# Kernel tuning notes

Hardware: AMD Instinct MI355X
Metric: run time of the kernel (lower is better)

Reference implementation:

```python
import jax, jax.numpy as jnp
import numpy as np

D_MODEL = 1024
N_HEADS = 16
D_HEAD = D_MODEL // N_HEADS
B, T = 4, 2048


def setup_inputs() -> dict:
    key = jax.random.key(0)
    ks = jax.random.split(key, 9)
    s = 0.02
    return {
        "x": jax.random.normal(ks[0], (B, T, D_MODEL), dtype=jnp.float32),
        "Wq": jax.random.normal(ks[1], (D_MODEL, D_MODEL), dtype=jnp.float32) * s,
        "bq": jnp.zeros((D_MODEL,), dtype=jnp.float32),
        "Wk": jax.random.normal(ks[2], (D_MODEL, D_MODEL), dtype=jnp.float32) * s,
        "bk": jnp.zeros((D_MODEL,), dtype=jnp.float32),
        "Wv": jax.random.normal(ks[3], (D_MODEL, D_MODEL), dtype=jnp.float32) * s,
        "bv": jnp.zeros((D_MODEL,), dtype=jnp.float32),
        "Wo": jax.random.normal(ks[4], (D_MODEL, D_MODEL), dtype=jnp.float32) * s,
        "bo": jnp.zeros((D_MODEL,), dtype=jnp.float32),
    }


def reference(x, Wq, bq, Wk, bk, Wv, bv, Wo, bo):
    # Dropout in eval mode (identity), as standard for a correctness baseline.
    Bx, Tx, _ = x.shape
    # torch nn.Linear: y = x @ W.T + b
    Q = x @ Wq.T + bq
    K = x @ Wk.T + bk
    V = x @ Wv.T + bv
    # [B, T, H, Dh] -> [B, H, T, Dh]
    Q = Q.reshape(Bx, Tx, N_HEADS, D_HEAD).transpose(0, 2, 1, 3)
    K = K.reshape(Bx, Tx, N_HEADS, D_HEAD).transpose(0, 2, 1, 3)
    V = V.reshape(Bx, Tx, N_HEADS, D_HEAD).transpose(0, 2, 1, 3)
    scale = 1.0 / jnp.sqrt(jnp.float32(D_HEAD))
    scores = jnp.einsum("bhqd,bhkd->bhqk", Q, K) * scale  # [B,H,T,T]
    # additive causal mask: -1e6 above the diagonal (matches torch.triu trick)
    mask = jnp.triu(jnp.full((Tx, Tx), -1000000.0, dtype=scores.dtype), k=1)
    scores = scores + mask
    attn = jax.nn.softmax(scores, axis=-1)
    out = jnp.einsum("bhqk,bhkd->bhqd", attn, V)  # [B,H,T,Dh]
    out = out.transpose(0, 2, 1, 3).reshape(Bx, Tx, D_MODEL)
    out = out @ Wo.T + bo
    return out
```

## Files before the change

### kernel.cpp

```cpp
#include <hip/hip_runtime.h>
#include <stdint.h>

#define DM 1024
#define HEADS 16
#define DH 64
#define BQ 4
#define TT 2048
#define MTOT (BQ*TT)
#define NQT (TT/64)

typedef __attribute__((ext_vector_type(8))) __bf16 bf16x8;
typedef __attribute__((ext_vector_type(4))) float f32x4;
typedef __attribute__((ext_vector_type(4))) uint32_t u32x4;
typedef unsigned short u16;
typedef __attribute__((ext_vector_type(8))) unsigned short u16x8;

__device__ __forceinline__ u16 f2b(float f) {
  uint32_t u = __builtin_bit_cast(uint32_t, f);
  u = (u + 0x7fffu + ((u >> 16) & 1u)) >> 16;
  return (u16)u;
}

__device__ __forceinline__ uint32_t cvtpk(float lo, float hi) {
  uint32_t r;
  asm("v_cvt_pk_bf16_f32 %0, %1, %2" : "=v"(r) : "v"(lo), "v"(hi));
  return r;
}

__device__ __forceinline__ void gload_lds16(const u16* g, u16* l) {
  __builtin_amdgcn_global_load_lds(
      (const __attribute__((address_space(1))) void*)g,
      (__attribute__((address_space(3))) void*)l, 16, 0, 0);
}

#define NX (MTOT * DM / 4)
#define NW (DM * DM / 4)
__global__ __launch_bounds__(256) void cast_all(const float* __restrict__ x,
                                                const float* __restrict__ Wq,
                                                const float* __restrict__ Wk,
                                                const float* __restrict__ Wv,
                                                const float* __restrict__ Wo,
                                                u16* __restrict__ xb,
                                                u16* __restrict__ wqkvb,
                                                u16* __restrict__ wob) {
  int i = blockIdx.x * 256 + threadIdx.x;
  const float* src; u16* dst;
  if (i < NX)               { src = x;  dst = xb; }
  else if (i < NX + NW)     { src = Wq; dst = wqkvb;          i -= NX; }
  else if (i < NX + 2 * NW) { src = Wk; dst = wqkvb + 4 * NW; i -= NX + NW; }
  else if (i < NX + 3 * NW) { src = Wv; dst = wqkvb + 8 * NW; i -= NX + 2 * NW; }
  else                      { src = Wo; dst = wob;            i -= NX + 3 * NW; }
  float4 v = ((const float4*)src)[i];
  ushort4 o;
  o.x = f2b(v.x); o.y = f2b(v.y); o.z = f2b(v.z); o.w = f2b(v.w);
  ((ushort4*)dst)[i] = o;
}

#define NK2 16
#define SLOT_A2 (256 * 64)
#define SLOT_B2 (128 * 64)
#define SLOT_E2 (SLOT_A2 + SLOT_B2)

__global__ __launch_bounds__(512, 2) void gemm_qkv8(const u16* __restrict__ A,
                                                    const u16* __restrict__ W,
                                                    const float* __restrict__ bq,
                                                    const float* __restrict__ bk,
                                                    const float* __restrict__ bv,
                                                    u16* __restrict__ Qo,
                                                    u16* __restrict__ Ko,
                                                    u16* __restrict__ Vto,
                                                    float qs) {
  __shared__ u16 lds[3 * SLOT_E2];
  const int tid = threadIdx.x, lane = tid & 63, wave = tid >> 6;
  const int fr = lane & 15, g = lane >> 4;
  const int wm = wave >> 1, wn = wave & 1;

  int bid = blockIdx.x;
  bid = (bid & 7) * 96 + (bid >> 3);
  const int by = bid / 24, bx = bid % 24;
  const int m0 = by * 256, n0 = bx * 128;

  const int lr8 = lane >> 3;
  const int lsc = ((lane & 7) ^ lr8) * 8;
  const u16* gA0 = A + (size_t)(m0 + wave * 8 + lr8) * DM + lsc;
  const u16* gB0 = W + (size_t)(n0 + wave * 8 + lr8) * DM + lsc;
  const int dA0 = wave * 512;
  const int dB0 = SLOT_A2 + wave * 512;

#define STAGEQ(ls, kt) {                                     \
    const int ke = (kt) * 64;                                \
    gload_lds16(gA0 + ke,                (ls) + dA0);        \
    gload_lds16(gA0 + ke + (size_t)64  * DM, (ls) + dA0 + 4096);  \
    gload_lds16(gA0 + ke + (size_t)128 * DM, (ls) + dA0 + 8192);  \
    gload_lds16(gA0 + ke + (size_t)192 * DM, (ls) + dA0 + 12288); \
    gload_lds16(gB0 + ke,                (ls) + dB0);        \
    gload_lds16(gB0 + ke + (size_t)64  * DM, (ls) + dB0 + 4096); }

  const int rc0 = ((g) ^ (fr & 7)) * 8;
  const int rc1 = ((4 + g) ^ (fr & 7)) * 8;
  const int offA = (wm * 64 + fr) * 64;
  const int offB = SLOT_A2 + (wn * 64 + fr) * 64;

  f32x4 acc[4][4];
#pragma unroll
  for (int mi = 0; mi < 4; ++mi)
#pragma unroll
    for (int ni = 0; ni < 4; ++ni) acc[mi][ni] = (f32x4){0.f, 0.f, 0.f, 0.f};

  bf16x8 afA[8], bfA[8], afB[8], bfB[8];

#define READQ(AFv, BFv, ls) {                                \
    _Pragma("unroll")                                        \
    for (int mi = 0; mi < 4; ++mi) {                         \
      AFv[2 * mi]     = *(const bf16x8*)&(ls)[offA + mi * 1024 + rc0]; \
      AFv[2 * mi + 1] = *(const bf16x8*)&(ls)[offA + mi * 1024 + rc1]; \
    }                                                        \
    _Pragma("unroll")                                        \
    for (int ni = 0; ni < 4; ++ni) {                         \
      BFv[2 * ni]     = *(const bf16x8*)&(ls)[offB + ni * 1024 + rc0]; \
      BFv[2 * ni + 1] = *(const bf16x8*)&(ls)[offB + ni * 1024 + rc1]; \
    } }

#define MFMAQ(AFv, BFv) {                                    \
    __builtin_amdgcn_s_setprio(1);                           \
    _Pragma("unroll")                                        \
    for (int mi = 0; mi < 4; ++mi)                           \
      _Pragma("unroll")                                      \
      for (int ni = 0; ni < 4; ++ni) {                       \
        acc[mi][ni] = __builtin_amdgcn_mfma_f32_16x16x32_bf16(AFv[2 * mi], BFv[2 * ni], acc[mi][ni], 0, 0, 0); \
        acc[mi][ni] = __builtin_amdgcn_mfma_f32_16x16x32_bf16(AFv[2 * mi + 1], BFv[2 * ni + 1], acc[mi][ni], 0, 0, 0); \
      }                                                      \
    __builtin_amdgcn_s_setprio(0); }

#define QW6 asm volatile("s_waitcnt vmcnt(6)" ::: "memory"); \
            asm volatile("s_barrier" ::: "memory");
#define QW0 asm volatile("s_waitcnt vmcnt(0)" ::: "memory"); \
            asm volatile("s_barrier" ::: "memory");

  u16* p0 = &lds[0];
  u16* p1 = &lds[SLOT_E2];
  u16* p2 = &lds[2 * SLOT_E2];
  u16 *pCur = p0, *pNxt = p1, *pStg = p2;

  STAGEQ(p0, 0)
  STAGEQ(p1, 1)
  asm volatile("s_waitcnt vmcnt(6)" ::: "memory");
  asm volatile("s_barrier" ::: "memory");
  READQ(afA, bfA, p0)

  for (int kt = 0; kt < NK2 - 2; kt += 2) {
    STAGEQ(pStg, kt + 2)
    QW6
    READQ(afB, bfB, pNxt)
    MFMAQ(afA, bfA)
    { u16* t = pCur; pCur = pNxt; pNxt = pStg; pStg = t; }
    if (kt + 3 < NK2) { STAGEQ(pStg, kt + 3) }
    QW6
    READQ(afA, bfA, pNxt)
    MFMAQ(afB, bfB)
    { u16* t = pCur; pCur = pNxt; pNxt = pStg; pStg = t; }
  }
  QW0
  READQ(afB, bfB, pNxt)
  MFMAQ(afA, bfA)
  MFMAQ(afB, bfB)

  const int g4 = g * 4;
  const int seg = n0 >> 10;
  const int nbase = (n0 & 1023) + wn * 64 + fr;
  if (seg == 0) {
#pragma unroll
    for (int ni = 0; ni < 4; ++ni) {
      const int cgl = nbase + ni * 16;
      const float bb = bq[cgl];
      const int hh = cgl >> 6, d = cgl & 63;
#pragma unroll
      for (int mi = 0; mi < 4; ++mi) {
        const int m = m0 + wm * 64 + mi * 16 + g4;
        const int bi = m >> 11, t = m & 2047;
        u16* dst = &Qo[(((size_t)bi * HEADS + hh) * TT + t) * DH + d];
#pragma unroll
        for (int j = 0; j < 4; ++j)
          dst[(size_t)j * DH] = f2b((acc[mi][ni][j] + bb) * qs);
      }
    }
  } else if (seg == 1) {
#pragma unroll
    for (int ni = 0; ni < 4; ++ni) {
      const int cgl = nbase + ni * 16;
      const float bb = bk[cgl];
      const int hh = cgl >> 6, d = cgl & 63;
#pragma unroll
      for (int mi = 0; mi < 4; ++mi) {
        const int m = m0 + wm * 64 + mi * 16 + g4;
        const int bi = m >> 11, t = m & 2047;
        u16* dst = &Ko[(((size_t)bi * HEADS + hh) * TT + t) * DH + d];
#pragma unroll
        for (int j = 0; j < 4; ++j)
          dst[(size_t)j * DH] = f2b(acc[mi][ni][j] + bb);
      }
    }
  } else {
#pragma unroll
    for (int ni = 0; ni < 4; ++ni) {
      const int cgl = nbase + ni * 16;
      const float bb = bv[cgl];
      const int hh = cgl >> 6, d = cgl & 63;
#pragma unroll
      for (int mi = 0; mi < 4; ++mi) {
        const int m = m0 + wm * 64 + mi * 16 + g4;
        const int t0 = m & 2047, bi = m >> 11;
        const int w64 = t0 & 63;
        const int pos = (t0 & ~63) | (((w64 >> 5) & 1) << 5) | (((w64 >> 2) & 3) << 3) |
                        (((w64 >> 4) & 1) << 2);
        ushort4 o;
        o.x = f2b(acc[mi][ni][0] + bb);
        o.y = f2b(acc[mi][ni][1] + bb);
        o.z = f2b(acc[mi][ni][2] + bb);
        o.w = f2b(acc[mi][ni][3] + bb);
        *(ushort4*)&Vto[(((size_t)bi * HEADS + hh) * DH + d) * TT + pos] = o;
      }
    }
  }
#undef STAGEQ
#undef READQ
#undef MFMAQ
#undef QW6
#undef QW0
}

#define SLOT_OA (256 * 32)
#define SLOT_OB (128 * 32)
#define SLOT_OE (SLOT_OA + SLOT_OB)

__global__ __launch_bounds__(512, 2) void gemm_out8(const u16* __restrict__ A,
                                                    const u16* __restrict__ Bw,
                                                    const float* __restrict__ bias,
                                                    float* __restrict__ outp) {
  __shared__ u16 lds[4 * SLOT_OE];
  const int tid = threadIdx.x, lane = tid & 63, wave = tid >> 6;
  const int fr = lane & 15, g = lane >> 4;
  const int wm = wave >> 1, wn = wave & 1;

  const int bx = blockIdx.x >> 5, by = blockIdx.x & 31;
  const int m0 = by * 256, n0 = bx * 128;

  const int srow = tid >> 2;
  const int schunk = (tid & 3) ^ ((tid >> 3) & 3);
  const u16* gA0 = A + (size_t)(m0 + srow) * DM + schunk * 8;
  const u16* gA1 = gA0 + (size_t)128 * DM;
  const u16* gB0 = Bw + (size_t)(n0 + srow) * DM + schunk * 8;
  const int dA0 = wave * 512;
  const int dA1 = 4096 + wave * 512;
  const int dB0 = SLOT_OA + wave * 512;

#define STAGEO(slot, kt) {                                   \
    u16* ls = &lds[(slot) * SLOT_OE];                        \
    const int ke = (kt) * 32;                                \
    gload_lds16(gA0 + ke, ls + dA0);                         \
    gload_lds16(gA1 + ke, ls + dA1);                         \
    gload_lds16(gB0 + ke, ls + dB0); }

  const int rchunk = (g ^ ((fr >> 1) & 3)) * 8;
  const int offA = (wm * 64 + fr) * 32 + rchunk;
  const int offB = SLOT_OA + (wn * 64 + fr) * 32 + rchunk;

  f32x4 acc[4][4];
#pragma unroll
  for (int mi = 0; mi < 4; ++mi)
#pragma unroll
    for (int ni = 0; ni < 4; ++ni) acc[mi][ni] = (f32x4){0.f, 0.f, 0.f, 0.f};

  bf16x8 afA[4], bfA[4], afB[4], bfB[4];

#define READO(AFv, BFv, kt) {                                \
    const u16* sl = &lds[((kt) & 3) * SLOT_OE];              \
    _Pragma("unroll")                                        \
    for (int mi = 0; mi < 4; ++mi)                           \
      AFv[mi] = *(const bf16x8*)&sl[offA + mi * 512];        \
    _Pragma("unroll")                                        \
    for (int ni = 0; ni < 4; ++ni)                           \
      BFv[ni] = *(const bf16x8*)&sl[offB + ni * 512]; }

#define MFMAO(AFv, BFv) {                                    \
    __builtin_amdgcn_s_setprio(1);                           \
    _Pragma("unroll")                                        \
    for (int mi = 0; mi < 4; ++mi)                           \
      _Pragma("unroll")                                      \
      for (int ni = 0; ni < 4; ++ni)                         \
        acc[mi][ni] = __builtin_amdgcn_mfma_f32_16x16x32_bf16(AFv[mi], BFv[ni], acc[mi][ni], 0, 0, 0); \
    __builtin_amdgcn_s_setprio(0); }

#define OW3 asm volatile("s_waitcnt vmcnt(3)" ::: "memory"); \
            asm volatile("s_barrier" ::: "memory");
#define OW0 asm volatile("s_waitcnt vmcnt(0)" ::: "memory"); \
            asm volatile("s_barrier" ::: "memory");

  STAGEO(0, 0)
  STAGEO(1, 1)
  STAGEO(2, 2)
  asm volatile("s_waitcnt vmcnt(6)" ::: "memory");
  asm volatile("s_barrier" ::: "memory");
  READO(afA, bfA, 0)

  for (int kt = 0; kt < 28; kt += 2) {
    OW3
    READO(afB, bfB, kt + 1)
    MFMAO(afA, bfA)
    STAGEO((kt + 3) & 3, kt + 3)
    OW3
    READO(afA, bfA, kt + 2)
    MFMAO(afB, bfB)
    STAGEO((kt + 4) & 3, kt + 4)
  }
  OW3
  READO(afB, bfB, 29)
  MFMAO(afA, bfA)
  STAGEO(3, 31)
  OW3
  READO(afA, bfA, 30)
  MFMAO(afB, bfB)
  OW0
  READO(afB, bfB, 31)
  MFMAO(afA, bfA)
  MFMAO(afB, bfB)

  const int g4 = g * 4;
#pragma unroll
  for (int mi = 0; mi < 4; ++mi) {
    const int rg = m0 + wm * 64 + mi * 16 + g4;
#pragma unroll
    for (int ni = 0; ni < 4; ++ni) {
      const int cg = n0 + wn * 64 + ni * 16 + fr;
      const float bb = bias[cg];
#pragma unroll
      for (int j = 0; j < 4; ++j)
        outp[(size_t)(rg + j) * DM + cg] = acc[mi][ni][j] + bb;
    }
  }
#undef STAGEO
#undef READO
#undef MFMAO
#undef OW3
#undef OW0
}

__global__ __launch_bounds__(256) void attn_fwd(const u16* __restrict__ Q,
                                                const u16* __restrict__ K,
                                                const u16* __restrict__ Vt,
                                                u16* __restrict__ O) {
  const int o_ = blockIdx.x;
  const int xcd = o_ & 7, j = o_ >> 3;
  const int gi = j & 7;
  const int qt128 = 15 - (j >> 3);
  const int gidx = xcd * 8 + gi;
  const int b = gidx >> 4, h = gidx & 15;
  const int tid = threadIdx.x, lane = tid & 63, wave = tid >> 6;
  __shared__ u16 Ks[64 * 64];
  __shared__ u16 Vs[64 * 64];

  const size_t bh = ((size_t)b * HEADS + h) * TT;
  const size_t vbse = ((size_t)b * HEADS + h) * DH;
  const int fr = lane & 15, g = lane >> 4;
  const int sr = tid >> 2;
  const int sc0 = tid & 3;

  const int sw1 = (sc0 ^ (sr & 7)) * 8;
  const int sw2 = ((sc0 + 4) ^ (sr & 7)) * 8;
  const int sgc = sc0 * 8;
  const int rk0 = (g ^ (fr & 7)) * 8;
  const int rk1 = ((4 + g) ^ (fr & 7)) * 8;
  const int k8 = g * 8;

  const int q0 = qt128 * 128;
  const int qtL = 2 * qt128, qtH = qtL + 1;
  const int qrowL = q0 + wave * 16 + fr;
  const int qrowH = q0 + 64 + wave * 16 + fr;
  const bf16x8 qfL0 = *(const bf16x8*)&Q[(bh + qrowL) * DH + k8];
  const bf16x8 qfL1 = *(const bf16x8*)&Q[(bh + qrowL) * DH + 32 + k8];
  const bf16x8 qfH0 = *(const bf16x8*)&Q[(bh + qrowH) * DH + k8];
  const bf16x8 qfH1 = *(const bf16x8*)&Q[(bh + qrowH) * DH + 32 + k8];

  float lsumL = 0.f, lsumH = 0.f;
  f32x4 oaccL[4], oaccH[4];
#pragma unroll
  for (int c = 0; c < 4; ++c) {
    oaccL[c] = (f32x4){0.f, 0.f, 0.f, 0.f};
    oaccH[c] = (f32x4){0.f, 0.f, 0.f, 0.f};
  }

  for (int kvb = 0; kvb <= qtH; ++kvb) {
    const int kv0 = kvb * 64;
    {
      const u16* kg = &K[(bh + kv0 + sr) * DH + sgc];
      u16x8 ka = *(const u16x8*)kg;
      u16x8 kc = *(const u16x8*)(kg + 32);
      const u16* vg = &Vt[(vbse + sr) * TT + kv0 + sgc];
      u16x8 va = *(const u16x8*)vg;
      u16x8 vc = *(const u16x8*)(vg + 32);
      *(u16x8*)&Ks[sr * 64 + sw1] = ka;
      *(u16x8*)&Ks[sr * 64 + sw2] = kc;
      *(u16x8*)&Vs[sr * 64 + sw1] = va;
      *(u16x8*)&Vs[sr * 64 + sw2] = vc;
    }
    __syncthreads();

    f32x4 sL[4], sH[4];
    __builtin_amdgcn_s_setprio(1);
#pragma unroll
    for (int c = 0; c < 4; ++c) {
      bf16x8 kb0 = *(const bf16x8*)&Ks[(c * 16 + fr) * 64 + rk0];
      bf16x8 kb1 = *(const bf16x8*)&Ks[(c * 16 + fr) * 64 + rk1];
      f32x4 tL = (f32x4){0.f, 0.f, 0.f, 0.f};
      tL = __builtin_amdgcn_mfma_f32_16x16x32_bf16(kb0, qfL0, tL, 0, 0, 0);
      tL = __builtin_amdgcn_mfma_f32_16x16x32_bf16(kb1, qfL1, tL, 0, 0, 0);
      sL[c] = tL;
      f32x4 tH = (f32x4){0.f, 0.f, 0.f, 0.f};
      tH = __builtin_amdgcn_mfma_f32_16x16x32_bf16(kb0, qfH0, tH, 0, 0, 0);
      tH = __builtin_amdgcn_mfma_f32_16x16x32_bf16(kb1, qfH1, tH, 0, 0, 0);
      sH[c] = tH;
    }
    __builtin_amdgcn_s_setprio(0);

    if (kvb >= qtL) {
#pragma unroll
      for (int c = 0; c < 4; ++c) {
        const int colg = kv0 + c * 16 + 4 * g;
#pragma unroll
        for (int r = 0; r < 4; ++r) {
          if (colg + r > qrowL) sL[c][r] = -1e30f;
          if (colg + r > qrowH) sH[c][r] = -1e30f;
        }
      }
    }

    float rsL = 0.f, rsH = 0.f;
    uint32_t pkL[8], pkH[8];
#pragma unroll
    for (int c = 0; c < 4; ++c) {
      float l0 = __builtin_amdgcn_exp2f(sL[c][0]);
      float l1 = __builtin_amdgcn_exp2f(sL[c][1]);
      float l2 = __builtin_amdgcn_exp2f(sL[c][2]);
      float l3 = __builtin_amdgcn_exp2f(sL[c][3]);
      rsL += (l0 + l1) + (l2 + l3);
      pkL[2 * c] = cvtpk(l0, l1);
      pkL[2 * c + 1] = cvtpk(l2, l3);
      float h0 = __builtin_amdgcn_exp2f(sH[c][0]);
      float h1 = __builtin_amdgcn_exp2f(sH[c][1]);
      float h2 = __builtin_amdgcn_exp2f(sH[c][2]);
      float h3 = __builtin_amdgcn_exp2f(sH[c][3]);
      rsH += (h0 + h1) + (h2 + h3);
      pkH[2 * c] = cvtpk(h0, h1);
      pkH[2 * c + 1] = cvtpk(h2, h3);
    }
    rsL += __shfl_xor(rsL, 16);
    rsL += __shfl_xor(rsL, 32);
    lsumL += rsL;
    rsH += __shfl_xor(rsH, 16);
    rsH += __shfl_xor(rsH, 32);
    lsumH += rsH;

    const bf16x8 paL0 = __builtin_bit_cast(bf16x8, (u32x4){pkL[0], pkL[1], pkL[2], pkL[3]});
    const bf16x8 paL1 = __builtin_bit_cast(bf16x8, (u32x4){pkL[4], pkL[5], pkL[6], pkL[7]});
    const bf16x8 paH0 = __builtin_bit_cast(bf16x8, (u32x4){pkH[0], pkH[1], pkH[2], pkH[3]});
    const bf16x8 paH1 = __builtin_bit_cast(bf16x8, (u32x4){pkH[4], pkH[5], pkH[6], pkH[7]});

    __builtin_amdgcn_s_setprio(1);
#pragma unroll
    for (int c = 0; c < 4; ++c) {
      bf16x8 vb0 = *(const bf16x8*)&Vs[(c * 16 + fr) * 64 + rk0];
      bf16x8 vb1 = *(const bf16x8*)&Vs[(c * 16 + fr) * 64 + rk1];
      oaccL[c] = __builtin_amdgcn_mfma_f32_16x16x32_bf16(vb0, paL0, oaccL[c], 0, 0, 0);
      oaccL[c] = __builtin_amdgcn_mfma_f32_16x16x32_bf16(vb1, paL1, oaccL[c], 0, 0, 0);
      oaccH[c] = __builtin_amdgcn_mfma_f32_16x16x32_bf16(vb0, paH0, oaccH[c], 0, 0, 0);
      oaccH[c] = __builtin_amdgcn_mfma_f32_16x16x32_bf16(vb1, paH1, oaccH[c], 0, 0, 0);
    }
    __builtin_amdgcn_s_setprio(0);
    __syncthreads();
  }

  const float invL = 1.f / lsumL;
#pragma unroll
  for (int c = 0; c < 4; ++c) {
    ushort4 o;
    o.x = f2b(oaccL[c][0] * invL);
    o.y = f2b(oaccL[c][1] * invL);
    o.z = f2b(oaccL[c][2] * invL);
    o.w = f2b(oaccL[c][3] * invL);
    *(ushort4*)&O[((size_t)b * TT + qrowL) * DM + h * DH + c * 16 + 4 * g] = o;
  }
  const float invH = 1.f / lsumH;
#pragma unroll
  for (int c = 0; c < 4; ++c) {
    ushort4 o;
    o.x = f2b(oaccH[c][0] * invH);
    o.y = f2b(oaccH[c][1] * invH);
    o.z = f2b(oaccH[c][2] * invH);
    o.w = f2b(oaccH[c][3] * invH);
    *(ushort4*)&O[((size_t)b * TT + qrowH) * DM + h * DH + c * 16 + 4 * g] = o;
  }
}

extern "C" void kernel_launch(void* const* d_in, const int* in_sizes, int n_in,
                              void* d_out, int out_size, void* d_ws, size_t ws_size,
                              hipStream_t stream) {
  const float* x  = (const float*)d_in[0];
  const float* Wq = (const float*)d_in[1];
  const float* bq = (const float*)d_in[2];
  const float* Wk = (const float*)d_in[3];
  const float* bk = (const float*)d_in[4];
  const float* Wv = (const float*)d_in[5];
  const float* bv = (const float*)d_in[6];
  const float* Wo = (const float*)d_in[7];
  const float* bo = (const float*)d_in[8];

  char* w = (char*)d_ws;
  u16* xb    = (u16*)w; w += (size_t)MTOT * DM * 2;
  u16* Wqkvb = (u16*)w; w += (size_t)3 * DM * DM * 2;
  u16* Wob   = (u16*)w; w += (size_t)DM * DM * 2;
  u16* Qb    = (u16*)w; w += (size_t)MTOT * DM * 2;
  u16* Kb    = (u16*)w; w += (size_t)MTOT * DM * 2;
  u16* Vtb   = (u16*)w; w += (size_t)MTOT * DM * 2;
  u16* AOb   = (u16*)w; w += (size_t)MTOT * DM * 2;

  cast_all<<<(NX + 4 * NW) / 256, 256, 0, stream>>>(x, Wq, Wk, Wv, Wo, xb, Wqkvb, Wob);

  const float qs = 0.125f * 1.44269504f;
  gemm_qkv8<<<768, 512, 0, stream>>>(xb, Wqkvb, bq, bk, bv, Qb, Kb, Vtb, qs);

  attn_fwd<<<1024, 256, 0, stream>>>(Qb, Kb, Vtb, AOb);

  gemm_out8<<<256, 512, 0, stream>>>(AOb, Wob, bo, (float*)d_out);
}
```

Before: 155.6 us.

## Double-buffer K/V tiles in attention with register prefetch of next block

The attention kernel now uses two LDS buffers for K and V and prefetches the next 64-key block from global memory into registers while the current block is being computed. The loop is unrolled by two, which removes one barrier per block. The goal is to hide global load latency behind the MFMA and exp work. In exchange it doubles the shared memory footprint and raises register pressure, which could lower occupancy.

```diff
diff --git a/kernel.cpp b/kernel.cpp
--- a/kernel.cpp
+++ b/kernel.cpp
@@ -356,18 +356,21 @@
   const int gidx = xcd * 8 + gi;
   const int b = gidx >> 4, h = gidx & 15;
   const int tid = threadIdx.x, lane = tid & 63, wave = tid >> 6;
-  __shared__ u16 Ks[64 * 64];
-  __shared__ u16 Vs[64 * 64];
+  __shared__ u16 Ks[2][64 * 64];
+  __shared__ u16 Vs[2][64 * 64];
 
   const size_t bh = ((size_t)b * HEADS + h) * TT;
   const size_t vbse = ((size_t)b * HEADS + h) * DH;
   const int fr = lane & 15, g = lane >> 4;
-  const int sr = tid >> 2;
-  const int sc0 = tid & 3;
-
-  const int sw1 = (sc0 ^ (sr & 7)) * 8;
-  const int sw2 = ((sc0 + 4) ^ (sr & 7)) * 8;
-  const int sgc = sc0 * 8;
+
+  const int srow = wave * 16 + (lane & 15);
+  const int gp = lane >> 4;
+  const int wc0 = (gp ^ (srow & 7)) * 8;
+  const int wc1 = ((gp + 4) ^ (srow & 7)) * 8;
+  const int ldw = srow * 64;
+  const u16* kRow = &K[(bh + srow) * DH + gp * 8];
+  const u16* vRow = &Vt[(vbse + srow) * TT + gp * 8];
+
   const int rk0 = (g ^ (fr & 7)) * 8;
   const int rk1 = ((4 + g) ^ (fr & 7)) * 8;
   const int k8 = g * 8;
@@ -389,94 +392,102 @@
     oaccH[c] = (f32x4){0.f, 0.f, 0.f, 0.f};
   }
 
-  for (int kvb = 0; kvb <= qtH; ++kvb) {
-    const int kv0 = kvb * 64;
-    {
-      const u16* kg = &K[(bh + kv0 + sr) * DH + sgc];
-      u16x8 ka = *(const u16x8*)kg;
-      u16x8 kc = *(const u16x8*)(kg + 32);
-      const u16* vg = &Vt[(vbse + sr) * TT + kv0 + sgc];
-      u16x8 va = *(const u16x8*)vg;
-      u16x8 vc = *(const u16x8*)(vg + 32);
-      *(u16x8*)&Ks[sr * 64 + sw1] = ka;
-      *(u16x8*)&Ks[sr * 64 + sw2] = kc;
-      *(u16x8*)&Vs[sr * 64 + sw1] = va;
-      *(u16x8*)&Vs[sr * 64 + sw2] = vc;
-    }
+#define LOADKV(KA, KC, VA, VC, kv0) {                       \
+    KA = *(const u16x8*)(kRow + (size_t)(kv0) * DH);        \
+    KC = *(const u16x8*)(kRow + (size_t)(kv0) * DH + 32);   \
+    VA = *(const u16x8*)(vRow + (kv0));                     \
+    VC = *(const u16x8*)(vRow + (kv0) + 32); }
+
+#define WRITEKV(BUF, KA, KC, VA, VC) {                      \
+    *(u16x8*)&Ks[BUF][ldw + wc0] = KA;                      \
+    *(u16x8*)&Ks[BUF][ldw + wc1] = KC;                      \
+    *(u16x8*)&Vs[BUF][ldw + wc0] = VA;                      \
+    *(u16x8*)&Vs[BUF][ldw + wc1] = VC; }
+
+#define COMPUTE_T(BUF, kvb) {                                                  \
+    f32x4 sL[4], sH[4];                                                        \
+    __builtin_amdgcn_s_setprio(1);                                             \
+    _Pragma("unroll")                                                          \
+    for (int c = 0; c < 4; ++c) {                                              \
+      bf16x8 kb0 = *(const bf16x8*)&Ks[BUF][(c * 16 + fr) * 64 + rk0];         \
+      bf16x8 kb1 = *(const bf16x8*)&Ks[BUF][(c * 16 + fr) * 64 + rk1];         \
+      f32x4 tL = (f32x4){0.f, 0.f, 0.f, 0.f};                                  \
+      tL = __builtin_amdgcn_mfma_f32_16x16x32_bf16(kb0, qfL0, tL, 0, 0, 0);    \
+      tL = __builtin_amdgcn_mfma_f32_16x16x32_bf16(kb1, qfL1, tL, 0, 0, 0);    \
+      sL[c] = tL;                                                              \
+      f32x4 tH = (f32x4){0.f, 0.f, 0.f, 0.f};                                  \
+      tH = __builtin_amdgcn_mfma_f32_16x16x32_bf16(kb0, qfH0, tH, 0, 0, 0);    \
+      tH = __builtin_amdgcn_mfma_f32_16x16x32_bf16(kb1, qfH1, tH, 0, 0, 0);    \
+      sH[c] = tH;                                                              \
+    }                                                                          \
+    __builtin_amdgcn_s_setprio(0);                                             \
+    if ((kvb) >= qtL) {                                                        \
+      const int kvm = (kvb) * 64;                                              \
+      _Pragma("unroll")                                                        \
+      for (int c = 0; c < 4; ++c) {                                            \
+        const int colg = kvm + c * 16 + 4 * g;                                 \
+        _Pragma("unroll")                                                      \
+        for (int r = 0; r < 4; ++r) {                                          \
+          if (colg + r > qrowL) sL[c][r] = -1e30f;                             \
+          if (colg + r > qrowH) sH[c][r] = -1e30f;                             \
+        }                                                                      \
+      }                                                                        \
+    }                                                                          \
+    float rsL = 0.f, rsH = 0.f;                                                \
+    uint32_t pkL[8], pkH[8];                                                   \
+    _Pragma("unroll")                                                          \
+    for (int c = 0; c < 4; ++c) {                                              \
+      float l0 = __builtin_amdgcn_exp2f(sL[c][0]);                             \
+      float l1 = __builtin_amdgcn_exp2f(sL[c][1]);                             \
+      float l2 = __builtin_amdgcn_exp2f(sL[c][2]);                             \
+      float l3 = __builtin_amdgcn_exp2f(sL[c][3]);                             \
+      rsL += (l0 + l1) + (l2 + l3);                                            \
+      pkL[2 * c] = cvtpk(l0, l1);                                              \
+      pkL[2 * c + 1] = cvtpk(l2, l3);                                          \
+      float h0 = __builtin_amdgcn_exp2f(sH[c][0]);                             \
+      float h1 = __builtin_amdgcn_exp2f(sH[c][1]);                             \
+      float h2 = __builtin_amdgcn_exp2f(sH[c][2]);                             \
+      float h3 = __builtin_amdgcn_exp2f(sH[c][3]);                             \
+      rsH += (h0 + h1) + (h2 + h3);                                            \
+      pkH[2 * c] = cvtpk(h0, h1);                                              \
+      pkH[2 * c + 1] = cvtpk(h2, h3);                                          \
+    }                                                                          \
+    rsL += __shfl_xor(rsL, 16);                                                \
+    rsL += __shfl_xor(rsL, 32);                                                \
+    lsumL += rsL;                                                              \
+    rsH += __shfl_xor(rsH, 16);                                                \
+    rsH += __shfl_xor(rsH, 32);                                                \
+    lsumH += rsH;                                                              \
+    const bf16x8 paL0 = __builtin_bit_cast(bf16x8, (u32x4){pkL[0], pkL[1], pkL[2], pkL[3]}); \
+    const bf16x8 paL1 = __builtin_bit_cast(bf16x8, (u32x4){pkL[4], pkL[5], pkL[6], pkL[7]}); \
+    const bf16x8 paH0 = __builtin_bit_cast(bf16x8, (u32x4){pkH[0], pkH[1], pkH[2], pkH[3]}); \
+    const bf16x8 paH1 = __builtin_bit_cast(bf16x8, (u32x4){pkH[4], pkH[5], pkH[6], pkH[7]}); \
+    __builtin_amdgcn_s_setprio(1);                                             \
+    _Pragma("unroll")                                                          \
+    for (int c = 0; c < 4; ++c) {                                              \
+      bf16x8 vb0 = *(const bf16x8*)&Vs[BUF][(c * 16 + fr) * 64 + rk0];         \
+      bf16x8 vb1 = *(const bf16x8*)&Vs[BUF][(c * 16 + fr) * 64 + rk1];         \
+      oaccL[c] = __builtin_amdgcn_mfma_f32_16x16x32_bf16(vb0, paL0, oaccL[c], 0, 0, 0); \
+      oaccL[c] = __builtin_amdgcn_mfma_f32_16x16x32_bf16(vb1, paL1, oaccL[c], 0, 0, 0); \
+      oaccH[c] = __builtin_amdgcn_mfma_f32_16x16x32_bf16(vb0, paH0, oaccH[c], 0, 0, 0); \
+      oaccH[c] = __builtin_amdgcn_mfma_f32_16x16x32_bf16(vb1, paH1, oaccH[c], 0, 0, 0); \
+    }                                                                          \
+    __builtin_amdgcn_s_setprio(0);                                             \
+  }
+
+  u16x8 kaA, kcA, vaA, vcA, kaB, kcB, vaB, vcB;
+  LOADKV(kaA, kcA, vaA, vcA, 0)
+
+  for (int it = 0; it <= qt128; ++it) {
+    const int kvA = 2 * it, kvB = 2 * it + 1;
+    WRITEKV(0, kaA, kcA, vaA, vcA)
+    LOADKV(kaB, kcB, vaB, vcB, kvB * 64)
     __syncthreads();
-
-    f32x4 sL[4], sH[4];
-    __builtin_amdgcn_s_setprio(1);
-#pragma unroll
-    for (int c = 0; c < 4; ++c) {
-      bf16x8 kb0 = *(const bf16x8*)&Ks[(c * 16 + fr) * 64 + rk0];
-      bf16x8 kb1 = *(const bf16x8*)&Ks[(c * 16 + fr) * 64 + rk1];
-      f32x4 tL = (f32x4){0.f, 0.f, 0.f, 0.f};
-      tL = __builtin_amdgcn_mfma_f32_16x16x32_bf16(kb0, qfL0, tL, 0, 0, 0);
-      tL = __builtin_amdgcn_mfma_f32_16x16x32_bf16(kb1, qfL1, tL, 0, 0, 0);
-      sL[c] = tL;
-      f32x4 tH = (f32x4){0.f, 0.f, 0.f, 0.f};
-      tH = __builtin_amdgcn_mfma_f32_16x16x32_bf16(kb0, qfH0, tH, 0, 0, 0);
-      tH = __builtin_amdgcn_mfma_f32_16x16x32_bf16(kb1, qfH1, tH, 0, 0, 0);
-      sH[c] = tH;
-    }
-    __builtin_amdgcn_s_setprio(0);
-
-    if (kvb >= qtL) {
-#pragma unroll
-      for (int c = 0; c < 4; ++c) {
-        const int colg = kv0 + c * 16 + 4 * g;
-#pragma unroll
-        for (int r = 0; r < 4; ++r) {
-          if (colg + r > qrowL) sL[c][r] = -1e30f;
-          if (colg + r > qrowH) sH[c][r] = -1e30f;
-        }
-      }
-    }
-
-    float rsL = 0.f, rsH = 0.f;
-    uint32_t pkL[8], pkH[8];
-#pragma unroll
-    for (int c = 0; c < 4; ++c) {
-      float l0 = __builtin_amdgcn_exp2f(sL[c][0]);
-      float l1 = __builtin_amdgcn_exp2f(sL[c][1]);
-      float l2 = __builtin_amdgcn_exp2f(sL[c][2]);
-      float l3 = __builtin_amdgcn_exp2f(sL[c][3]);
-      rsL += (l0 + l1) + (l2 + l3);
-      pkL[2 * c] = cvtpk(l0, l1);
-      pkL[2 * c + 1] = cvtpk(l2, l3);
-      float h0 = __builtin_amdgcn_exp2f(sH[c][0]);
-      float h1 = __builtin_amdgcn_exp2f(sH[c][1]);
-      float h2 = __builtin_amdgcn_exp2f(sH[c][2]);
-      float h3 = __builtin_amdgcn_exp2f(sH[c][3]);
-      rsH += (h0 + h1) + (h2 + h3);
-      pkH[2 * c] = cvtpk(h0, h1);
-      pkH[2 * c + 1] = cvtpk(h2, h3);
-    }
-    rsL += __shfl_xor(rsL, 16);
-    rsL += __shfl_xor(rsL, 32);
-    lsumL += rsL;
-    rsH += __shfl_xor(rsH, 16);
-    rsH += __shfl_xor(rsH, 32);
-    lsumH += rsH;
-
-    const bf16x8 paL0 = __builtin_bit_cast(bf16x8, (u32x4){pkL[0], pkL[1], pkL[2], pkL[3]});
-    const bf16x8 paL1 = __builtin_bit_cast(bf16x8, (u32x4){pkL[4], pkL[5], pkL[6], pkL[7]});
-    const bf16x8 paH0 = __builtin_bit_cast(bf16x8, (u32x4){pkH[0], pkH[1], pkH[2], pkH[3]});
-    const bf16x8 paH1 = __builtin_bit_cast(bf16x8, (u32x4){pkH[4], pkH[5], pkH[6], pkH[7]});
-
-    __builtin_amdgcn_s_setprio(1);
-#pragma unroll
-    for (int c = 0; c < 4; ++c) {
-      bf16x8 vb0 = *(const bf16x8*)&Vs[(c * 16 + fr) * 64 + rk0];
-      bf16x8 vb1 = *(const bf16x8*)&Vs[(c * 16 + fr) * 64 + rk1];
-      oaccL[c] = __builtin_amdgcn_mfma_f32_16x16x32_bf16(vb0, paL0, oaccL[c], 0, 0, 0);
-      oaccL[c] = __builtin_amdgcn_mfma_f32_16x16x32_bf16(vb1, paL1, oaccL[c], 0, 0, 0);
-      oaccH[c] = __builtin_amdgcn_mfma_f32_16x16x32_bf16(vb0, paH0, oaccH[c], 0, 0, 0);
-      oaccH[c] = __builtin_amdgcn_mfma_f32_16x16x32_bf16(vb1, paH1, oaccH[c], 0, 0, 0);
-    }
-    __builtin_amdgcn_s_setprio(0);
+    COMPUTE_T(0, kvA)
+    WRITEKV(1, kaB, kcB, vaB, vcB)
+    if (it < qt128) LOADKV(kaA, kcA, vaA, vcA, (kvB + 1) * 64)
     __syncthreads();
+    COMPUTE_T(1, kvB)
   }
 
   const float invL = 1.f / lsumL;
@@ -499,6 +510,9 @@
     o.w = f2b(oaccH[c][3] * invH);
     *(ushort4*)&O[((size_t)b * TT + qrowH) * DM + h * DH + c * 16 + 4 * g] = o;
   }
+#undef LOADKV
+#undef WRITEKV
+#undef COMPUTE_T
 }
 
 extern "C" void kernel_launch(void* const* d_in, const int* in_sizes, int n_in,
```

Result: slower. 161.5 us (+3.8%).
